# Kernel optimization log

Hardware: AMD Instinct MI355X
Metric: run time of the kernel (lower is better)

The kernel has to match this reference:

```python
import jax, jax.numpy as jnp
import numpy as np

N = 50000      # query points
M = 50000      # support points
H = 32         # max neighbors
K = 15         # kernel points
CIN = 64
COUT = 128
KP_EXTENT = 0.06
RADIUS = 0.05


def setup_inputs() -> dict:
    key = jax.random.key(0)
    k1, k2, k3, k4, k5, k6, k7 = jax.random.split(key, 7)
    # point coordinates in a small cube so neighbors fall within KP_extent of kernel points
    q_pts = jax.random.uniform(k1, (N, 3), dtype=jnp.float32) * 0.1
    s_pts = jax.random.uniform(k2, (M, 3), dtype=jnp.float32) * 0.1
    # indices in [0, M]; index M selects the shadow (padded) support point
    neighb_inds = jax.random.randint(k3, (N, H), 0, M + 1)
    x = jax.random.normal(k4, (M, CIN), dtype=jnp.float32)
    # kaiming-uniform-like init for [K, Cin, Cout] weights
    weights = jax.random.normal(k5, (K, CIN, COUT), dtype=jnp.float32) / np.sqrt(CIN)
    # kernel points uniformly in a sphere of radius RADIUS, center point fixed at origin
    d = jax.random.normal(k6, (K, 3), dtype=jnp.float32)
    d = d / jnp.linalg.norm(d, axis=1, keepdims=True)
    r = jax.random.uniform(k7, (K, 1), dtype=jnp.float32) ** (1.0 / 3.0) * RADIUS
    kernel_points = (d * r).at[0].set(0.0)
    return {"q_pts": q_pts, "s_pts": s_pts, "x": x, "weights": weights,
            "kernel_points": kernel_points, "neighb_inds": neighb_inds}


def reference(q_pts, s_pts, x, weights, kernel_points, neighb_inds):
    # pad support points with a far-away shadow point (matches torch: +1e6)
    s_pad = jnp.concatenate([s_pts, jnp.full((1, s_pts.shape[1]), 1e6, s_pts.dtype)], axis=0)
    # gather neighbor coords and center on queries: [N, H, 3]
    neighbors = s_pad[neighb_inds] - q_pts[:, None, :]
    # squared distances to each kernel point: [N, H, K]
    diff = neighbors[:, :, None, :] - kernel_points[None, None, :, :]
    sq_d = jnp.sum(diff * diff, axis=3)
    # linear influence, transposed to [N, K, H]
    h = jnp.maximum(1.0 - jnp.sqrt(sq_d) / KP_EXTENT, 0.0)
    h = jnp.swapaxes(h, 1, 2)
    # pad features with a zero row for shadow neighbors, then gather: [N, H, Cin]
    x_pad = jnp.concatenate([x, jnp.zeros((1, x.shape[1]), x.dtype)], axis=0)
    neighb_x = x_pad[neighb_inds]
    # project features onto kernel points: [N, K, Cin]
    fpk = jnp.einsum('nkh,nhc->nkc', h, neighb_x)
    # per-kernel-point matmul + sum over kernel points: [N, Cout]
    out = jnp.einsum('nkc,kco->no', fpk, weights)
    return out
```

## Files before the change

kernel.cpp:

```cpp
#include <hip/hip_runtime.h>

#define NQ     50000
#define MS     50000
#define NH     32
#define NK     15
#define CIN    64
#define COUT   128
#define QT     16
#define INV_EXT (1.0f/0.06f)

typedef unsigned int   uint32;
typedef unsigned short u16;
typedef _Float16 f16;
typedef _Float16 f16x8 __attribute__((ext_vector_type(8)));
typedef float    f32x4 __attribute__((ext_vector_type(4)));

#define WB_BYTES  (8*32*64*8*2)
#define XPH_BYTES (MS*CIN*2)

#if __has_builtin(__builtin_amdgcn_sqrtf)
#define SQRTF __builtin_amdgcn_sqrtf
#else
#define SQRTF sqrtf
#endif

__device__ __forceinline__ uint32 permlo(uint32 A, uint32 B) {
#if __has_builtin(__builtin_amdgcn_perm)
    return __builtin_amdgcn_perm(A, B, 0x01000504u);
#else
    return (A & 0xffffu) | (B << 16);
#endif
}
__device__ __forceinline__ uint32 permhi(uint32 A, uint32 B) {
#if __has_builtin(__builtin_amdgcn_perm)
    return __builtin_amdgcn_perm(A, B, 0x03020706u);
#else
    return (A >> 16) | (B & 0xffff0000u);
#endif
}

__device__ __forceinline__ u16 f16bits(float f) {
    return __builtin_bit_cast(u16, (f16)f);
}

__device__ __forceinline__ uint32 pk2(float a, float b) {
#if __has_builtin(__builtin_amdgcn_cvt_pkrtz)
    return __builtin_bit_cast(uint32, __builtin_amdgcn_cvt_pkrtz(a, b));
#else
    return (uint32)f16bits(a) | ((uint32)f16bits(b) << 16);
#endif
}

__device__ __forceinline__ uint32 swA(uint32 o) {
    return o ^ ((((o >> 11) & 7u) ^ ((o >> 7) & 1u)) << 4);
}

__global__ __launch_bounds__(256)
void pack_all(const float* __restrict__ x, u16* __restrict__ xph,
              const float* __restrict__ w, u16* __restrict__ wb) {
    const int bid = blockIdx.x;
    if (bid < 3125) {
        const int tid = bid * 256 + threadIdx.x;
        const int row = tid >> 4;
        const int lp  = tid & 15;
        const float v0 = x[row*CIN +  0 + lp];
        const float v1 = x[row*CIN + 16 + lp];
        const float v2 = x[row*CIN + 32 + lp];
        const float v3 = x[row*CIN + 48 + lp];
        uint2 d;
        d.x = pk2(v0, v1);
        d.y = pk2(v2, v3);
        *(uint2*)&xph[row*CIN + lp*4] = d;
    } else {
        const int u  = (bid - 3125) * 4 + (threadIdx.x >> 6);
        const int nt = u >> 5;
        const int ks = u & 31;
        const int l  = threadIdx.x & 63;
        u16 frag[8];
        #pragma unroll
        for (int e = 0; e < 8; ++e) {
            const int Kp = ks*32 + (l >> 4)*8 + e;
            const int c  = Kp >> 4;
            const int k  = Kp & 15;
            const float val = (k < NK) ? w[(k*CIN + c)*COUT + nt*16 + (l & 15)] : 0.0f;
            frag[e] = f16bits(val);
        }
        *(f16x8*)&wb[((nt*32 + ks)*64 + l)*8] = *(f16x8*)frag;
    }
}

__global__ __launch_bounds__(256, 4)
void kpconv_fused(const float* __restrict__ q_pts,
                  const float* __restrict__ s_pts,
                  const u16*  __restrict__ xph,
                  const u16*  __restrict__ wb,
                  const float* __restrict__ kp,
                  const int*   __restrict__ nind,
                  float* __restrict__ out)
{
    __shared__ u16   fpkAT[QT*1024];
    __shared__ float nb[QT*100];
    __shared__ u16   inds[QT*NH];

    const int t  = threadIdx.x;
    const int q0 = blockIdx.x * QT;

    #pragma unroll
    for (int p = t; p < QT*NH; p += 256) {
        const int q = p >> 5, j = p & 31;
        const int ind = nind[(q0 + q)*NH + j];
        const bool valid = (ind < MS);
        inds[p] = (u16)(valid ? ind : 0);
        float sx, sy, sz;
        if (valid) { sx = s_pts[ind*3+0]; sy = s_pts[ind*3+1]; sz = s_pts[ind*3+2]; }
        else       { sx = 1e6f; sy = 1e6f; sz = 1e6f; }
        nb[q*100 + j*3 + 0] = sx - q_pts[(q0+q)*3+0];
        nb[q*100 + j*3 + 1] = sy - q_pts[(q0+q)*3+1];
        nb[q*100 + j*3 + 2] = sz - q_pts[(q0+q)*3+2];
    }
    __syncthreads();

    {
        const int l  = t & 63, wv = t >> 6;
        const int lc = l & 15, lg = l >> 4;
        const int kc = (lc < NK) ? lc : (NK - 1);
        const float kx = kp[kc*3+0], ky = kp[kc*3+1], kz = kp[kc*3+2];

        uint2 v[4][8];
        #pragma unroll
        for (int qi = 0; qi < 4; ++qi) {
            const int q = wv*4 + qi;
            const uint4 iv = *(const uint4*)&inds[q*NH + lg*8];
            uint32 r[8];
            r[0] = iv.x & 0xffffu; r[1] = iv.x >> 16;
            r[2] = iv.y & 0xffffu; r[3] = iv.y >> 16;
            r[4] = iv.z & 0xffffu; r[5] = iv.z >> 16;
            r[6] = iv.w & 0xffffu; r[7] = iv.w >> 16;
            #pragma unroll
            for (int e = 0; e < 8; ++e)
                v[qi][e] = *(const uint2*)(xph + r[e]*CIN + lc*4);
        }

        #pragma unroll
        for (int qi = 0; qi < 4; ++qi) {
            const int q = wv*4 + qi;
            const float* nbq = &nb[q*100 + lg*24];
            const float4 r0 = *(const float4*)(nbq +  0);
            const float4 r1 = *(const float4*)(nbq +  4);
            const float4 r2 = *(const float4*)(nbq +  8);
            const float4 r3 = *(const float4*)(nbq + 12);
            const float4 r4 = *(const float4*)(nbq + 16);
            const float4 r5 = *(const float4*)(nbq + 20);
            float jx[8], jy[8], jz[8];
            jx[0]=r0.x; jy[0]=r0.y; jz[0]=r0.z;
            jx[1]=r0.w; jy[1]=r1.x; jz[1]=r1.y;
            jx[2]=r1.z; jy[2]=r1.w; jz[2]=r2.x;
            jx[3]=r2.y; jy[3]=r2.z; jz[3]=r2.w;
            jx[4]=r3.x; jy[4]=r3.y; jz[4]=r3.z;
            jx[5]=r3.w; jy[5]=r4.x; jz[5]=r4.y;
            jx[6]=r4.z; jy[6]=r4.w; jz[6]=r5.x;
            jx[7]=r5.y; jy[7]=r5.z; jz[7]=r5.w;
            float hh[8];
            #pragma unroll
            for (int e = 0; e < 8; ++e) {
                const float dx = jx[e] - kx;
                const float dy = jy[e] - ky;
                const float dz = jz[e] - kz;
                float h = 1.0f - SQRTF(dx*dx + dy*dy + dz*dz) * INV_EXT;
                hh[e] = (h > 0.0f) ? h : 0.0f;
            }
            uint32 ab[4];
            ab[0] = pk2(hh[0], hh[1]); ab[1] = pk2(hh[2], hh[3]);
            ab[2] = pk2(hh[4], hh[5]); ab[3] = pk2(hh[6], hh[7]);
            const f16x8 a = __builtin_bit_cast(f16x8, *(uint4*)ab);
            f32x4 acc0 = {0,0,0,0}, acc1 = {0,0,0,0}, acc2 = {0,0,0,0}, acc3 = {0,0,0,0};
            #pragma unroll
            for (int ct = 0; ct < 4; ++ct) {
                const uint32 A0 = (ct & 2) ? v[qi][0].y : v[qi][0].x, B0 = (ct & 2) ? v[qi][1].y : v[qi][1].x;
                const uint32 A1 = (ct & 2) ? v[qi][2].y : v[qi][2].x, B1 = (ct & 2) ? v[qi][3].y : v[qi][3].x;
                const uint32 A2 = (ct & 2) ? v[qi][4].y : v[qi][4].x, B2 = (ct & 2) ? v[qi][5].y : v[qi][5].x;
                const uint32 A3 = (ct & 2) ? v[qi][6].y : v[qi][6].x, B3 = (ct & 2) ? v[qi][7].y : v[qi][7].x;
                uint4 bd;
                if (ct & 1) {
                    bd.x = permhi(A0, B0); bd.y = permhi(A1, B1);
                    bd.z = permhi(A2, B2); bd.w = permhi(A3, B3);
                } else {
                    bd.x = permlo(A0, B0); bd.y = permlo(A1, B1);
                    bd.z = permlo(A2, B2); bd.w = permlo(A3, B3);
                }
                const f16x8 b = __builtin_bit_cast(f16x8, bd);
                if      (ct == 0) acc0 = __builtin_amdgcn_mfma_f32_16x16x32_f16(a, b, acc0, 0,0,0);
                else if (ct == 1) acc1 = __builtin_amdgcn_mfma_f32_16x16x32_f16(a, b, acc1, 0,0,0);
                else if (ct == 2) acc2 = __builtin_amdgcn_mfma_f32_16x16x32_f16(a, b, acc2, 0,0,0);
                else              acc3 = __builtin_amdgcn_mfma_f32_16x16x32_f16(a, b, acc3, 0,0,0);
            }
            #pragma unroll
            for (int ct = 0; ct < 4; ++ct) {
                const f32x4 av = (ct==0)?acc0:(ct==1)?acc1:(ct==2)?acc2:acc3;
                uint2 dv;
                dv.x = pk2(av[0], av[1]);
                dv.y = pk2(av[2], av[3]);
                const uint32 o = swA((uint32)(q*2048 + (ct*16 + lc)*32 + lg*8));
                *(uint2*)((char*)fpkAT + o) = dv;
            }
        }
    }
    __syncthreads();

    {
        const int l   = t & 63;
        const int w   = t >> 6;
        const int col = l & 15;
        const int kg  = l >> 4;
        const int nt0 = w * 2;
        f32x4 acc0 = {0.f,0.f,0.f,0.f};
        f32x4 acc1 = {0.f,0.f,0.f,0.f};
        const u16* b0p = wb + (nt0*32)*512 + l*8;
        const u16* b1p = b0p + 32*512;
        const uint32 abase = (uint32)(col*2048 + kg*16);
        #pragma unroll 8
        for (int ks = 0; ks < 32; ++ks) {
            const uint32 aoff = swA(abase + (uint32)(ks*64));
            const f16x8 a  = *(const f16x8*)((const char*)fpkAT + aoff);
            const f16x8 b0 = *(const f16x8*)(b0p + ks*512);
            const f16x8 b1 = *(const f16x8*)(b1p + ks*512);
            acc0 = __builtin_amdgcn_mfma_f32_16x16x32_f16(a, b0, acc0, 0, 0, 0);
            acc1 = __builtin_amdgcn_mfma_f32_16x16x32_f16(a, b1, acc1, 0, 0, 0);
        }
        const int rbase = kg * 4;
        #pragma unroll
        for (int r = 0; r < 4; ++r) {
            out[(q0 + rbase + r)*COUT + nt0*16 + col]      = acc0[r];
            out[(q0 + rbase + r)*COUT + nt0*16 + 16 + col] = acc1[r];
        }
    }
}

extern "C" void kernel_launch(void* const* d_in, const int* in_sizes, int n_in,
                              void* d_out, int out_size, void* d_ws, size_t ws_size,
                              hipStream_t stream) {
    const float* q_pts = (const float*)d_in[0];
    const float* s_pts = (const float*)d_in[1];
    const float* x     = (const float*)d_in[2];
    const float* wts   = (const float*)d_in[3];
    const float* kp    = (const float*)d_in[4];
    const int*   nind  = (const int*)d_in[5];
    float* out = (float*)d_out;

    u16* wbp = (u16*)d_ws;
    u16* xph = (u16*)((char*)d_ws + WB_BYTES);

    hipLaunchKernelGGL(pack_all, dim3(3125 + 64), dim3(256), 0, stream, x, xph, wts, wbp);
    hipLaunchKernelGGL(kpconv_fused, dim3(NQ/QT), dim3(256), 0, stream,
                       q_pts, s_pts, xph, wbp, kp, nind, out);
}
```

Baseline: 67.24 us.

## Double query tile to 32 with 512-thread blocks and prefetch weight fragments

Raises the per-block query tile from 16 to 32 and the block size from 256 to 512 threads. Each wave now owns one 16-column output tile for both 16-row query halves, so every weight fragment it loads serves two MFMAs. The first four weight fragments are loaded before the barrier to hide global latency. Bounds guards handle the partial last block, since 50000 is not a multiple of 32. The cost is larger shared memory per block and fewer blocks, which may reduce occupancy.

```diff
diff --git a/kernel.cpp b/kernel.cpp
--- a/kernel.cpp
+++ b/kernel.cpp
@@ -6,7 +6,7 @@
 #define NK     15
 #define CIN    64
 #define COUT   128
-#define QT     16
+#define QT     32
 #define INV_EXT (1.0f/0.06f)
 
 typedef unsigned int   uint32;
@@ -89,7 +89,7 @@
     }
 }
 
-__global__ __launch_bounds__(256, 4)
+__global__ __launch_bounds__(512, 4)
 void kpconv_fused(const float* __restrict__ q_pts,
                   const float* __restrict__ s_pts,
                   const u16*  __restrict__ xph,
@@ -106,17 +106,19 @@
     const int q0 = blockIdx.x * QT;
 
     #pragma unroll
-    for (int p = t; p < QT*NH; p += 256) {
+    for (int p = t; p < QT*NH; p += 512) {
         const int q = p >> 5, j = p & 31;
-        const int ind = nind[(q0 + q)*NH + j];
+        const int qg = q0 + q;
+        const int qc = (qg < NQ) ? qg : (NQ - 1);
+        const int ind = nind[qc*NH + j];
         const bool valid = (ind < MS);
         inds[p] = (u16)(valid ? ind : 0);
         float sx, sy, sz;
         if (valid) { sx = s_pts[ind*3+0]; sy = s_pts[ind*3+1]; sz = s_pts[ind*3+2]; }
         else       { sx = 1e6f; sy = 1e6f; sz = 1e6f; }
-        nb[q*100 + j*3 + 0] = sx - q_pts[(q0+q)*3+0];
-        nb[q*100 + j*3 + 1] = sy - q_pts[(q0+q)*3+1];
-        nb[q*100 + j*3 + 2] = sz - q_pts[(q0+q)*3+2];
+        nb[q*100 + j*3 + 0] = sx - q_pts[qc*3+0];
+        nb[q*100 + j*3 + 1] = sy - q_pts[qc*3+1];
+        nb[q*100 + j*3 + 2] = sz - q_pts[qc*3+2];
     }
     __syncthreads();
 
@@ -205,33 +207,47 @@
             }
         }
     }
+
+    const int l   = t & 63;
+    const int nt  = t >> 6;
+    const u16* bp = wb + (nt*32)*512 + l*8;
+    uint4 pb0 = *(const uint4*)(bp + 0*512);
+    uint4 pb1 = *(const uint4*)(bp + 1*512);
+    uint4 pb2 = *(const uint4*)(bp + 2*512);
+    uint4 pb3 = *(const uint4*)(bp + 3*512);
+
     __syncthreads();
 
     {
-        const int l   = t & 63;
-        const int w   = t >> 6;
         const int col = l & 15;
         const int kg  = l >> 4;
-        const int nt0 = w * 2;
         f32x4 acc0 = {0.f,0.f,0.f,0.f};
         f32x4 acc1 = {0.f,0.f,0.f,0.f};
-        const u16* b0p = wb + (nt0*32)*512 + l*8;
-        const u16* b1p = b0p + 32*512;
-        const uint32 abase = (uint32)(col*2048 + kg*16);
+        const uint32 abase0 = (uint32)(col*2048 + kg*16);
+        const uint32 abase1 = abase0 + 16*2048;
         #pragma unroll 8
         for (int ks = 0; ks < 32; ++ks) {
-            const uint32 aoff = swA(abase + (uint32)(ks*64));
-            const f16x8 a  = *(const f16x8*)((const char*)fpkAT + aoff);
-            const f16x8 b0 = *(const f16x8*)(b0p + ks*512);
-            const f16x8 b1 = *(const f16x8*)(b1p + ks*512);
-            acc0 = __builtin_amdgcn_mfma_f32_16x16x32_f16(a, b0, acc0, 0, 0, 0);
-            acc1 = __builtin_amdgcn_mfma_f32_16x16x32_f16(a, b1, acc1, 0, 0, 0);
+            const uint32 aoff0 = swA(abase0 + (uint32)(ks*64));
+            const uint32 aoff1 = swA(abase1 + (uint32)(ks*64));
+            const f16x8 a0 = *(const f16x8*)((const char*)fpkAT + aoff0);
+            const f16x8 a1 = *(const f16x8*)((const char*)fpkAT + aoff1);
+            uint4 bd;
+            if      (ks == 0) bd = pb0;
+            else if (ks == 1) bd = pb1;
+            else if (ks == 2) bd = pb2;
+            else if (ks == 3) bd = pb3;
+            else              bd = *(const uint4*)(bp + ks*512);
+            const f16x8 b = __builtin_bit_cast(f16x8, bd);
+            acc0 = __builtin_amdgcn_mfma_f32_16x16x32_f16(a0, b, acc0, 0, 0, 0);
+            acc1 = __builtin_amdgcn_mfma_f32_16x16x32_f16(a1, b, acc1, 0, 0, 0);
         }
         const int rbase = kg * 4;
         #pragma unroll
         for (int r = 0; r < 4; ++r) {
-            out[(q0 + rbase + r)*COUT + nt0*16 + col]      = acc0[r];
-            out[(q0 + rbase + r)*COUT + nt0*16 + 16 + col] = acc1[r];
+            const int row0 = q0 + rbase + r;
+            const int row1 = row0 + 16;
+            if (row0 < NQ) out[row0*COUT + nt*16 + col] = acc0[r];
+            if (row1 < NQ) out[row1*COUT + nt*16 + col] = acc1[r];
         }
     }
 }
@@ -251,6 +267,6 @@
     u16* xph = (u16*)((char*)d_ws + WB_BYTES);
 
     hipLaunchKernelGGL(pack_all, dim3(3125 + 64), dim3(256), 0, stream, x, xph, wts, wbp);
-    hipLaunchKernelGGL(kpconv_fused, dim3(NQ/QT), dim3(256), 0, stream,
+    hipLaunchKernelGGL(kpconv_fused, dim3((NQ + QT - 1) / QT), dim3(512), 0, stream,
                        q_pts, s_pts, xph, wbp, kp, nind, out);
 }
```

Measured after the change: 64.56 us. 4.0% less time.

## Double block size to 512 threads and prefetch weight fragments before barrier

Applied to the files above, without the earlier changes.

Raises the fused kernel's block from 256 to 512 threads. Each wave now handles 2 queries instead of 4 in the feature-projection phase and one 16-column output tile instead of two in the final GEMM. The first four weight fragments are loaded before the barrier so they overlap with waiting on other waves. This is meant to add latency hiding and parallelism per block, at the cost of more register and barrier pressure per block and half as much work per wave.

```diff
diff --git a/kernel.cpp b/kernel.cpp
--- a/kernel.cpp
+++ b/kernel.cpp
@@ -89,7 +89,7 @@
     }
 }
 
-__global__ __launch_bounds__(256, 4)
+__global__ __launch_bounds__(512, 4)
 void kpconv_fused(const float* __restrict__ q_pts,
                   const float* __restrict__ s_pts,
                   const u16*  __restrict__ xph,
@@ -105,8 +105,8 @@
     const int t  = threadIdx.x;
     const int q0 = blockIdx.x * QT;
 
-    #pragma unroll
-    for (int p = t; p < QT*NH; p += 256) {
+    {
+        const int p = t;
         const int q = p >> 5, j = p & 31;
         const int ind = nind[(q0 + q)*NH + j];
         const bool valid = (ind < MS);
@@ -126,10 +126,10 @@
         const int kc = (lc < NK) ? lc : (NK - 1);
         const float kx = kp[kc*3+0], ky = kp[kc*3+1], kz = kp[kc*3+2];
 
-        uint2 v[4][8];
-        #pragma unroll
-        for (int qi = 0; qi < 4; ++qi) {
-            const int q = wv*4 + qi;
+        uint2 v[2][8];
+        #pragma unroll
+        for (int qi = 0; qi < 2; ++qi) {
+            const int q = wv*2 + qi;
             const uint4 iv = *(const uint4*)&inds[q*NH + lg*8];
             uint32 r[8];
             r[0] = iv.x & 0xffffu; r[1] = iv.x >> 16;
@@ -142,8 +142,8 @@
         }
 
         #pragma unroll
-        for (int qi = 0; qi < 4; ++qi) {
-            const int q = wv*4 + qi;
+        for (int qi = 0; qi < 2; ++qi) {
+            const int q = wv*2 + qi;
             const float* nbq = &nb[q*100 + lg*24];
             const float4 r0 = *(const float4*)(nbq +  0);
             const float4 r1 = *(const float4*)(nbq +  4);
@@ -205,34 +205,39 @@
             }
         }
     }
+
+    const int l  = t & 63;
+    const int nt = t >> 6;
+    const u16* bp = wb + (nt*32)*512 + l*8;
+    uint4 pb0 = *(const uint4*)(bp + 0*512);
+    uint4 pb1 = *(const uint4*)(bp + 1*512);
+    uint4 pb2 = *(const uint4*)(bp + 2*512);
+    uint4 pb3 = *(const uint4*)(bp + 3*512);
+
     __syncthreads();
 
     {
-        const int l   = t & 63;
-        const int w   = t >> 6;
         const int col = l & 15;
         const int kg  = l >> 4;
-        const int nt0 = w * 2;
         f32x4 acc0 = {0.f,0.f,0.f,0.f};
-        f32x4 acc1 = {0.f,0.f,0.f,0.f};
-        const u16* b0p = wb + (nt0*32)*512 + l*8;
-        const u16* b1p = b0p + 32*512;
         const uint32 abase = (uint32)(col*2048 + kg*16);
         #pragma unroll 8
         for (int ks = 0; ks < 32; ++ks) {
             const uint32 aoff = swA(abase + (uint32)(ks*64));
-            const f16x8 a  = *(const f16x8*)((const char*)fpkAT + aoff);
-            const f16x8 b0 = *(const f16x8*)(b0p + ks*512);
-            const f16x8 b1 = *(const f16x8*)(b1p + ks*512);
-            acc0 = __builtin_amdgcn_mfma_f32_16x16x32_f16(a, b0, acc0, 0, 0, 0);
-            acc1 = __builtin_amdgcn_mfma_f32_16x16x32_f16(a, b1, acc1, 0, 0, 0);
+            const f16x8 a = *(const f16x8*)((const char*)fpkAT + aoff);
+            uint4 bd;
+            if      (ks == 0) bd = pb0;
+            else if (ks == 1) bd = pb1;
+            else if (ks == 2) bd = pb2;
+            else if (ks == 3) bd = pb3;
+            else              bd = *(const uint4*)(bp + ks*512);
+            const f16x8 b = __builtin_bit_cast(f16x8, bd);
+            acc0 = __builtin_amdgcn_mfma_f32_16x16x32_f16(a, b, acc0, 0, 0, 0);
         }
         const int rbase = kg * 4;
         #pragma unroll
-        for (int r = 0; r < 4; ++r) {
-            out[(q0 + rbase + r)*COUT + nt0*16 + col]      = acc0[r];
-            out[(q0 + rbase + r)*COUT + nt0*16 + 16 + col] = acc1[r];
-        }
+        for (int r = 0; r < 4; ++r)
+            out[(q0 + rbase + r)*COUT + nt*16 + col] = acc0[r];
     }
 }
 
@@ -251,6 +256,6 @@
     u16* xph = (u16*)((char*)d_ws + WB_BYTES);
 
     hipLaunchKernelGGL(pack_all, dim3(3125 + 64), dim3(256), 0, stream, x, xph, wts, wbp);
-    hipLaunchKernelGGL(kpconv_fused, dim3(NQ/QT), dim3(256), 0, stream,
+    hipLaunchKernelGGL(kpconv_fused, dim3(NQ/QT), dim3(512), 0, stream,
                        q_pts, s_pts, xph, wbp, kp, nind, out);
 }
```

New measurement: 68.20 us. About the same (+1.4%).
